# Kernel optimization log

Hardware: AMD Instinct MI355X
Metric: run time of the kernel (lower is better)

Reference implementation:

```python
import jax, jax.numpy as jnp
import numpy as np


def _conv(x, w, b, dilation=1):
    # NHWC input, HWIO kernel, SAME padding, optional dilation (TF Conv2D semantics)
    y = jax.lax.conv_general_dilated(
        x, w, window_strides=(1, 1), padding='SAME',
        rhs_dilation=(dilation, dilation),
        dimension_numbers=('NHWC', 'HWIO', 'NHWC'))
    return y + b


def _grid_pool(x, row_loc, col_loc):
    # Irregular-grid mean pool + broadcast back (tf resize of a 1x1 cell == broadcast).
    # Vectorized as two normalized one-hot contractions instead of per-cell loops.
    B, H, W, C = x.shape
    M = row_loc.shape[0] - 1
    N = col_loc.shape[0] - 1
    row_ids = jnp.searchsorted(row_loc, jnp.arange(H), side='right') - 1  # [H] in [0,M)
    col_ids = jnp.searchsorted(col_loc, jnp.arange(W), side='right') - 1  # [W] in [0,N)
    Rm = jax.nn.one_hot(row_ids, M, dtype=x.dtype).T            # [M,H]
    Cm = jax.nn.one_hot(col_ids, N, dtype=x.dtype)              # [W,N]
    Rm = Rm / jnp.sum(Rm, axis=1, keepdims=True)                # row-mean weights
    Cm = Cm / jnp.sum(Cm, axis=0, keepdims=True)                # col-mean weights
    pooled = jnp.einsum('mh,bhwc,wn->bmnc', Rm, x, Cm)          # per-cell means [B,M,N,C]
    return pooled[:, row_ids][:, :, col_ids]                    # broadcast back [B,H,W,C]


def setup_inputs() -> dict:
    key = jax.random.key(0)
    ks = jax.random.split(key, 8)
    B, H, W, Cin = 2, 1024, 1024, 18
    inp = {
        'input': jax.random.normal(ks[0], (B, H, W, Cin), dtype=jnp.float32),
        'row_loc': (jnp.arange(17, dtype=jnp.int32) * (H // 16)),  # 16 irregular-capable cells, endpoints 0..H
        'col_loc': (jnp.arange(17, dtype=jnp.int32) * (W // 16)),
        'w1': jax.random.normal(ks[1], (3, 3, Cin, 6), dtype=jnp.float32) * 0.1,
        'b1': jnp.zeros((6,), jnp.float32),
        'w2': jax.random.normal(ks[2], (3, 3, Cin, 6), dtype=jnp.float32) * 0.1,
        'b2': jnp.zeros((6,), jnp.float32),
        'w3': jax.random.normal(ks[3], (3, 3, Cin, 6), dtype=jnp.float32) * 0.1,
        'b3': jnp.zeros((6,), jnp.float32),
        'wb1': jax.random.normal(ks[4], (1, 1, 18, 18), dtype=jnp.float32) * 0.1,
        'bb1': jnp.zeros((18,), jnp.float32),
        'wb2': jax.random.normal(ks[5], (1, 1, 18, 1), dtype=jnp.float32) * 0.1,
        'bb2': jnp.zeros((1,), jnp.float32),
    }
    return inp


def reference(input, row_loc, col_loc, w1, b1, w2, b2, w3, b3, wb1, bb1, wb2, bb2):
    c1 = jax.nn.relu(_conv(input, w1, b1, 1))
    c2 = jax.nn.relu(_conv(input, w2, b2, 2))
    c3 = jax.nn.relu(_conv(input, w3, b3, 3))
    c = jnp.concatenate([c1, c2, c3], axis=3)          # [B,H,W,18]
    branch1 = jax.nn.relu(_conv(c, wb1, bb1, 1))       # [B,H,W,18]
    branch1 = _grid_pool(branch1, row_loc, col_loc)
    branch2 = _conv(c, wb2, bb2, 1)                    # [B,H,W,1]
    branch2 = _grid_pool(branch2, row_loc, col_loc)
    branch2 = jax.nn.sigmoid(branch2)
    output = jnp.concatenate([branch1, c, branch2], axis=3)  # [B,H,W,37]
    return (output, branch2)
```

## Files before the change

### kernel.cpp

```cpp
#include <hip/hip_runtime.h>
#include <math.h>

typedef _Float16 f16;
typedef _Float16 f16x2 __attribute__((ext_vector_type(2)));
typedef _Float16 f16x8 __attribute__((ext_vector_type(8)));
typedef float    f32x4 __attribute__((ext_vector_type(4)));

static constexpr int B = 2, H = 1024, W = 1024;
static constexpr int NCELL = 16;
static constexpr unsigned TOTAL1 = 2u*1024u*1024u*37u;

static constexpr size_t WT_OFF   = 0;
static constexpr size_t WBT_OFF  = 21504;
static constexpr size_t BIAS_OFF = 23552;
static constexpr size_t CWS_OFF  = 32768;
static constexpr size_t SUMS_OFF = CWS_OFF + (size_t)8192*9216;
static constexpr size_t P1_OFF   = SUMS_OFF + 9728*4;
static constexpr size_t P2_OFF   = P1_OFF + 9216*4;
static constexpr size_t RID_OFF  = P2_OFF + 512*4;
static constexpr size_t CID_OFF  = RID_OFF + 1024*4;

__device__ __forceinline__ int cell_of(const int* __restrict__ loc, int x) {
    int id = 0;
#pragma unroll
    for (int i = 1; i < NCELL; ++i) id = (loc[i] <= x) ? i : id;
    return id;
}

__global__ __launch_bounds__(256)
void prep(const float* __restrict__ w1, const float* __restrict__ b1,
          const float* __restrict__ w2, const float* __restrict__ b2,
          const float* __restrict__ w3, const float* __restrict__ b3,
          const float* __restrict__ wb1, const float* __restrict__ bb1,
          const float* __restrict__ wb2, const float* __restrict__ bb2,
          f16* __restrict__ wT, f16* __restrict__ wbT, float* __restrict__ biasPad)
{
    const int tid = threadIdx.x;
    for (int t = tid; t < 10752; t += 256) {
        int cv = t / 3584, r = t - cv*3584;
        int co = r / 224,  k = r - co*224;
        float val = 0.f;
        if (k < 216 && co < 6) {
            int tap = k / 24, ci = k - tap*24;
            if (ci < 18) {
                const float* wsrc = cv==0 ? w1 : cv==1 ? w2 : w3;
                val = wsrc[(tap*18 + ci)*6 + co];
            }
        }
        wT[t] = (f16)val;
    }
    for (int t = tid; t < 1024; t += 256) {
        int nt = t >> 9, r = t & 511;
        int colv = r >> 5, ci = r & 31;
        int co2 = nt*16 + colv;
        float val = 0.f;
        if (ci < 18) {
            if (co2 < 18) val = wb1[ci*18 + co2];
            else if (co2 == 18) val = wb2[ci];
        }
        wbT[t] = (f16)val;
    }
    for (int t = tid; t < 80; t += 256) {
        float val = 0.f;
        if (t < 48) { int cv = t >> 4, co = t & 15;
            const float* bp = cv==0 ? b1 : cv==1 ? b2 : b3;
            val = (co < 6) ? bp[co] : 0.f; }
        else if (t < 64) val = bb1[t - 48];
        else { int c = t - 64;
            val = (c==0) ? bb1[16] : (c==1) ? bb1[17] : (c==2) ? bb2[0] : 0.f; }
        biasPad[t] = val;
    }
}

__global__ __launch_bounds__(256)
void conv_mfma(const float* __restrict__ in,
               const f16* __restrict__ wT, const f16* __restrict__ wbT,
               const float* __restrict__ biasPad,
               const int* __restrict__ row_loc, const int* __restrict__ col_loc,
               f16* __restrict__ c_ws, float* __restrict__ sums)
{
    __shared__ __align__(16) f16 s_a[22*22*24];
    __shared__ float s_red[4][19];

    const int tid = threadIdx.x;
    const int bx  = blockIdx.x;
    const int b   = bx >> 12, rem = bx & 4095;
    const int h0  = (rem >> 6) * 16, w0 = (rem & 63) * 16;

    const int gh0 = h0 - 3, gw0 = w0 - 3;
    const bool interior = (gh0 >= 0) && (h0 + 19 <= H) && (gw0 >= 0) && (w0 + 19 <= W);
#pragma unroll
    for (int k = 0; k < 2; ++k) {
        const int p = tid + k*256;
        if (p < 484) {
            const int r = p / 22, cc = p - r*22;
            const int gh = gh0 + r, gw = gw0 + cc;
            const bool ok = interior || ((unsigned)gh < (unsigned)H && (unsigned)gw < (unsigned)W);
            float2 L[9];
            if (ok) {
                const float* sp = in + ((size_t)((size_t)b*H + gh)*W + gw)*18;
#pragma unroll
                for (int j = 0; j < 9; ++j) L[j] = *(const float2*)(sp + 2*j);
            } else {
#pragma unroll
                for (int j = 0; j < 9; ++j) L[j] = make_float2(0.f, 0.f);
            }
            f16x8 A0, A1, A2;
#pragma unroll
            for (int j = 0; j < 4; ++j) { A0[2*j] = (f16)L[j].x;   A0[2*j+1] = (f16)L[j].y; }
#pragma unroll
            for (int j = 0; j < 4; ++j) { A1[2*j] = (f16)L[4+j].x; A1[2*j+1] = (f16)L[4+j].y; }
            A2[0] = (f16)L[8].x; A2[1] = (f16)L[8].y;
#pragma unroll
            for (int j = 2; j < 8; ++j) A2[j] = (f16)0.f;
            *(f16x8*)&s_a[p*24 + 0]  = A0;
            *(f16x8*)&s_a[p*24 + 8]  = A1;
            *(f16x8*)&s_a[p*24 + 16] = A2;
        }
    }
    __syncthreads();

    const int lane = tid & 63, wv = tid >> 6;
    const int lm = lane & 15, g = lane >> 4;

    f32x4 acc[3][4];
#pragma unroll
    for (int cv = 0; cv < 3; ++cv)
#pragma unroll
        for (int mt = 0; mt < 4; ++mt) acc[cv][mt] = (f32x4){0.f,0.f,0.f,0.f};

#pragma unroll
    for (int cv = 0; cv < 3; ++cv) {
        const int d = cv + 1;
        const f16* wtc = wT + cv*3584 + lm*224 + g*8;
        f16x8 bf[7];
#pragma unroll
        for (int kb = 0; kb < 7; ++kb) bf[kb] = *(const f16x8*)(wtc + kb*32);
        int tofs[7];
#pragma unroll
        for (int kb = 0; kb < 7; ++kb) {
            int i8 = kb*4 + g; if (i8 > 26) i8 = 26;
            int tap = i8 / 3;
            int ci0 = (i8 - tap*3) * 8;
            int ky = tap / 3, kx = tap - ky*3;
            tofs[kb] = (((ky-1)*d)*22 + (kx-1)*d)*24 + ci0;
        }
#pragma unroll
        for (int mt = 0; mt < 4; ++mt) {
            const int py = wv*4 + mt;
            const int base = ((py + 3)*22 + lm + 3) * 24;
            f32x4 a = acc[cv][mt];
#pragma unroll
            for (int kb = 0; kb < 7; ++kb) {
                f16x8 af = *(const f16x8*)&s_a[base + tofs[kb]];
                a = __builtin_amdgcn_mfma_f32_16x16x32_f16(af, bf[kb], a, 0, 0, 0);
            }
            acc[cv][mt] = a;
        }
    }

    __syncthreads();
    f16* ct = s_a;
    const float bs0 = biasPad[lm], bs1 = biasPad[16 + lm], bs2 = biasPad[32 + lm];
    const bool act = (lm < 6);
#pragma unroll
    for (int cv = 0; cv < 3; ++cv) {
        const float bv = cv==0 ? bs0 : cv==1 ? bs1 : bs2;
#pragma unroll
        for (int mt = 0; mt < 4; ++mt) {
            const int py = wv*4 + mt;
#pragma unroll
            for (int r = 0; r < 4; ++r) {
                float val = fmaxf(acc[cv][mt][r] + bv, 0.f);
                const int px = g*4 + r;
                if (act) ct[(py*16 + px)*18 + cv*6 + lm] = (f16)val;
            }
        }
    }
    __syncthreads();

    {
        const f16x8* src = (const f16x8*)ct;
        f16x8* dst = (f16x8*)(c_ws + (size_t)bx * 4608);
#pragma unroll
        for (int k = 0; k < 3; ++k) {
            const int i = tid + k*256;
            if (i < 576) dst[i] = src[i];
        }
    }

    const f16x8 wbf0 = *(const f16x8*)(wbT + lm*32 + g*8);
    const f16x8 wbf1 = *(const f16x8*)(wbT + (16 + lm)*32 + g*8);
    const f32x4 z4 = (f32x4){0.f,0.f,0.f,0.f};
    const unsigned* ctu = (const unsigned*)ct;
    f32x4 acc2[4][2];
#pragma unroll
    for (int mt = 0; mt < 4; ++mt) {
        const int py = wv*4 + mt;
        const int du = ((py*16 + lm)*36 + g*16) >> 2;
        union { f16x8 v; unsigned u[4]; } A;
#pragma unroll
        for (int j = 0; j < 4; ++j) A.u[j] = ctu[du + j];
        acc2[mt][0] = __builtin_amdgcn_mfma_f32_16x16x32_f16(A.v, wbf0, z4, 0, 0, 0);
        acc2[mt][1] = __builtin_amdgcn_mfma_f32_16x16x32_f16(A.v, wbf1, z4, 0, 0, 0);
    }

    const float bb0 = biasPad[48 + lm];
    const float bb1v = biasPad[64 + lm];
    const int rid0 = cell_of(row_loc, h0), rid1 = cell_of(row_loc, h0 + 15);
    const int cid0 = cell_of(col_loc, w0), cid1 = cell_of(col_loc, w0 + 15);
    if (rid0 == rid1 && cid0 == cid1) {
        float ps0 = 0.f, ps1 = 0.f;
#pragma unroll
        for (int mt = 0; mt < 4; ++mt)
#pragma unroll
            for (int r = 0; r < 4; ++r) {
                float v0 = fmaxf(acc2[mt][0][r] + bb0, 0.f);
                float t1 = acc2[mt][1][r] + bb1v;
                float v1x = (lm < 2) ? fmaxf(t1, 0.f) : t1;
                ps0 += v0; ps1 += v1x;
            }
        ps0 += __shfl_xor(ps0, 16); ps0 += __shfl_xor(ps0, 32);
        ps1 += __shfl_xor(ps1, 16); ps1 += __shfl_xor(ps1, 32);
        if (lane < 16) s_red[wv][lane] = ps0;
        if (lane < 3)  s_red[wv][16 + lane] = ps1;
        __syncthreads();
        if (tid < 19) {
            float s = s_red[0][tid] + s_red[1][tid] + s_red[2][tid] + s_red[3][tid];
            const int cell = b*256 + rid0*16 + cid0;
            atomicAdd(&sums[cell*19 + tid], s);
        }
    } else {
#pragma unroll
        for (int mt = 0; mt < 4; ++mt) {
            const int py = wv*4 + mt;
            const int rid = cell_of(row_loc, h0 + py);
#pragma unroll
            for (int r = 0; r < 4; ++r) {
                const int px = g*4 + r;
                const int cell = b*256 + rid*16 + cell_of(col_loc, w0 + px);
                float v0 = fmaxf(acc2[mt][0][r] + bb0, 0.f);
                atomicAdd(&sums[cell*19 + lm], v0);
                if (lm < 3) {
                    float t1 = acc2[mt][1][r] + bb1v;
                    float v1x = (lm < 2) ? fmaxf(t1, 0.f) : t1;
                    atomicAdd(&sums[cell*19 + 16 + lm], v1x);
                }
            }
        }
    }
}

__global__ __launch_bounds__(256)
void finalize(const int* __restrict__ row_loc, const int* __restrict__ col_loc,
              const float* __restrict__ sums,
              float* __restrict__ pooled1, float* __restrict__ pooled2,
              int* __restrict__ row_ids, int* __restrict__ col_ids)
{
    __shared__ int rcnt[NCELL], ccnt[NCELL];
    const int tid = threadIdx.x;
    if (tid < NCELL) { rcnt[tid] = 0; ccnt[tid] = 0; }
    __syncthreads();
    for (int h = tid; h < H; h += 256) {
        int r = cell_of(row_loc, h); row_ids[h] = r; atomicAdd(&rcnt[r], 1);
    }
    for (int w = tid; w < W; w += 256) {
        int cc = cell_of(col_loc, w); col_ids[w] = cc; atomicAdd(&ccnt[cc], 1);
    }
    __syncthreads();
    for (int t = tid; t < B*256*18; t += 256) {
        int cell = t / 18, ch = t - cell*18;
        int rid = (cell >> 4) & 15, cid = cell & 15;
        int cnt = rcnt[rid] * ccnt[cid];
        pooled1[t] = (cnt > 0) ? sums[cell*19 + ch] / (float)cnt : 0.f;
    }
    for (int t = tid; t < B*256; t += 256) {
        int rid = (t >> 4) & 15, cid = t & 15;
        int cnt = rcnt[rid] * ccnt[cid];
        float v = (cnt > 0) ? sums[t*19 + 18] / (float)cnt : 0.f;
        pooled2[t] = 1.f / (1.f + __expf(-v));
    }
}

__global__ __launch_bounds__(256)
void assemble(const f16* __restrict__ c_ws, const float* __restrict__ pooled1,
              const float* __restrict__ pooled2, const int* __restrict__ row_ids,
              const int* __restrict__ col_ids, float* __restrict__ out)
{
    __shared__ __align__(16) f16 s_c[1024*18];
    __shared__ float s_p1[16*18];
    __shared__ float s_p2[16];
    __shared__ unsigned char s_cid[1024];

    const int tid = threadIdx.x;
    const int bx  = blockIdx.x;
    const int b   = bx >> 10, h = bx & 1023;

    const int tbase = b*4096 + (h >> 4)*64;
    const size_t rofs = (size_t)(h & 15) * 576;
    const char* cbase = (const char*)c_ws;
    float4* dstv = (float4*)s_c;
#pragma unroll
    for (int k = 0; k < 9; ++k) {
        const int j = tid + k*256;
        const int t = j / 36, i = j - t*36;
        const float4 v = *(const float4*)(cbase + (size_t)(tbase + t)*9216 + rofs + (size_t)i*16);
        dstv[j] = v;
    }
    const int rid = row_ids[h];
    for (int i = tid; i < 288; i += 256) {
        int cid = i / 18, ch = i - cid*18;
        s_p1[i] = pooled1[((size_t)(b*256 + rid*16 + cid))*18 + ch];
    }
    if (tid < 16) s_p2[tid] = pooled2[b*256 + rid*16 + tid];
    for (int i = tid; i < 1024; i += 256) s_cid[i] = (unsigned char)col_ids[i];
    __syncthreads();

    float* orow = out + (size_t)bx * (1024*37);
    for (int i4 = tid; i4 < 1024*37/4; i4 += 256) {
        const int o0 = i4*4;
        float v[4];
#pragma unroll
        for (int j = 0; j < 4; ++j) {
            const int o = o0 + j;
            const unsigned pix = (unsigned)o / 37u;
            const int ch = o - (int)pix*37;
            const int cid = s_cid[pix];
            float val;
            if (ch < 18)       val = s_p1[cid*18 + ch];
            else if (ch < 36)  val = (float)s_c[pix*18 + (ch - 18)];
            else               val = s_p2[cid];
            v[j] = val;
        }
        *(float4*)(orow + o0) = make_float4(v[0], v[1], v[2], v[3]);
    }
    float* o2 = out + (size_t)TOTAL1 + (size_t)bx * 1024;
    {
        const int p0 = tid * 4;
        float4 v = make_float4(s_p2[s_cid[p0]], s_p2[s_cid[p0+1]],
                               s_p2[s_cid[p0+2]], s_p2[s_cid[p0+3]]);
        *(float4*)(o2 + p0) = v;
    }
}

extern "C" void kernel_launch(void* const* d_in, const int* in_sizes, int n_in,
                              void* d_out, int out_size, void* d_ws, size_t ws_size,
                              hipStream_t stream)
{
    (void)in_sizes; (void)n_in; (void)out_size; (void)ws_size;
    const float* in      = (const float*)d_in[0];
    const int*   row_loc = (const int*)d_in[1];
    const int*   col_loc = (const int*)d_in[2];
    const float *w1 = (const float*)d_in[3],  *b1  = (const float*)d_in[4];
    const float *w2 = (const float*)d_in[5],  *b2  = (const float*)d_in[6];
    const float *w3 = (const float*)d_in[7],  *b3  = (const float*)d_in[8];
    const float *wb1= (const float*)d_in[9],  *bb1 = (const float*)d_in[10];
    const float *wb2= (const float*)d_in[11], *bb2 = (const float*)d_in[12];

    float* out = (float*)d_out;
    char*  ws  = (char*)d_ws;

    f16*   wT      = (f16*)(ws + WT_OFF);
    f16*   wbT     = (f16*)(ws + WBT_OFF);
    float* biasPad = (float*)(ws + BIAS_OFF);
    f16*   c_ws    = (f16*)(ws + CWS_OFF);
    float* sums    = (float*)(ws + SUMS_OFF);
    float* pooled1 = (float*)(ws + P1_OFF);
    float* pooled2 = (float*)(ws + P2_OFF);
    int*   row_ids = (int*)(ws + RID_OFF);
    int*   col_ids = (int*)(ws + CID_OFF);

    prep<<<dim3(1), dim3(256), 0, stream>>>(w1, b1, w2, b2, w3, b3,
                                            wb1, bb1, wb2, bb2, wT, wbT, biasPad);
    (void)hipMemsetAsync(sums, 0, 9728*sizeof(float), stream);

    conv_mfma<<<dim3(8192), dim3(256), 0, stream>>>(
        in, wT, wbT, biasPad, row_loc, col_loc, c_ws, sums);

    finalize<<<dim3(1), dim3(256), 0, stream>>>(
        row_loc, col_loc, sums, pooled1, pooled2, row_ids, col_ids);

    assemble<<<dim3(B*H), dim3(256), 0, stream>>>(
        c_ws, pooled1, pooled2, row_ids, col_ids, out);
}
```

Before: 210.9 us.

## Process four tiles per block with double-buffered register prefetch of halo loads

After: 413.4 us. +96.0%, slower.

```diff
diff --git a/kernel.cpp b/kernel.cpp
--- a/kernel.cpp
+++ b/kernel.cpp
@@ -9,6 +9,9 @@
 static constexpr int B = 2, H = 1024, W = 1024;
 static constexpr int NCELL = 16;
 static constexpr unsigned TOTAL1 = 2u*1024u*1024u*37u;
+
+static constexpr int NT_PER_BLK = 4;
+static constexpr int NBLK = 8192 / NT_PER_BLK;
 
 static constexpr size_t WT_OFF   = 0;
 static constexpr size_t WBT_OFF  = 21504;
@@ -27,15 +30,46 @@
     return id;
 }
 
+struct PxRegs { float2 v[9]; };
+
+__device__ __forceinline__ void issue_load(PxRegs& P, const float* __restrict__ in,
+                                           int b, int gh, int gw) {
+    const bool ok = ((unsigned)gh < (unsigned)H) && ((unsigned)gw < (unsigned)W);
+    if (ok) {
+        const float* sp = in + ((size_t)((size_t)b*H + gh)*W + gw)*18;
+#pragma unroll
+        for (int j = 0; j < 9; ++j) P.v[j] = *(const float2*)(sp + 2*j);
+    } else {
+#pragma unroll
+        for (int j = 0; j < 9; ++j) P.v[j] = make_float2(0.f, 0.f);
+    }
+}
+
+__device__ __forceinline__ void stage_write(f16* __restrict__ sa, const PxRegs& P, int p) {
+    f16x8 A0, A1, A2;
+#pragma unroll
+    for (int j = 0; j < 4; ++j) { A0[2*j] = (f16)P.v[j].x;   A0[2*j+1] = (f16)P.v[j].y; }
+#pragma unroll
+    for (int j = 0; j < 4; ++j) { A1[2*j] = (f16)P.v[4+j].x; A1[2*j+1] = (f16)P.v[4+j].y; }
+    A2[0] = (f16)P.v[8].x; A2[1] = (f16)P.v[8].y;
+#pragma unroll
+    for (int j = 2; j < 8; ++j) A2[j] = (f16)0.f;
+    *(f16x8*)&sa[p*24 + 0]  = A0;
+    *(f16x8*)&sa[p*24 + 8]  = A1;
+    *(f16x8*)&sa[p*24 + 16] = A2;
+}
+
 __global__ __launch_bounds__(256)
 void prep(const float* __restrict__ w1, const float* __restrict__ b1,
           const float* __restrict__ w2, const float* __restrict__ b2,
           const float* __restrict__ w3, const float* __restrict__ b3,
           const float* __restrict__ wb1, const float* __restrict__ bb1,
           const float* __restrict__ wb2, const float* __restrict__ bb2,
-          f16* __restrict__ wT, f16* __restrict__ wbT, float* __restrict__ biasPad)
+          f16* __restrict__ wT, f16* __restrict__ wbT, float* __restrict__ biasPad,
+          float* __restrict__ sums)
 {
     const int tid = threadIdx.x;
+    for (int t = tid; t < 9728; t += 256) sums[t] = 0.f;
     for (int t = tid; t < 10752; t += 256) {
         int cv = t / 3584, r = t - cv*3584;
         int co = r / 224,  k = r - co*224;
@@ -72,181 +106,174 @@
     }
 }
 
-__global__ __launch_bounds__(256)
+__global__ __launch_bounds__(256, 3)
 void conv_mfma(const float* __restrict__ in,
                const f16* __restrict__ wT, const f16* __restrict__ wbT,
                const float* __restrict__ biasPad,
                const int* __restrict__ row_loc, const int* __restrict__ col_loc,
                f16* __restrict__ c_ws, float* __restrict__ sums)
 {
-    __shared__ __align__(16) f16 s_a[22*22*24];
+    __shared__ __align__(16) f16 s_a[2][484*24];
     __shared__ float s_red[4][19];
 
     const int tid = threadIdx.x;
-    const int bx  = blockIdx.x;
-    const int b   = bx >> 12, rem = bx & 4095;
-    const int h0  = (rem >> 6) * 16, w0 = (rem & 63) * 16;
-
-    const int gh0 = h0 - 3, gw0 = w0 - 3;
-    const bool interior = (gh0 >= 0) && (h0 + 19 <= H) && (gw0 >= 0) && (w0 + 19 <= W);
-#pragma unroll
-    for (int k = 0; k < 2; ++k) {
-        const int p = tid + k*256;
-        if (p < 484) {
-            const int r = p / 22, cc = p - r*22;
-            const int gh = gh0 + r, gw = gw0 + cc;
-            const bool ok = interior || ((unsigned)gh < (unsigned)H && (unsigned)gw < (unsigned)W);
-            float2 L[9];
-            if (ok) {
-                const float* sp = in + ((size_t)((size_t)b*H + gh)*W + gw)*18;
-#pragma unroll
-                for (int j = 0; j < 9; ++j) L[j] = *(const float2*)(sp + 2*j);
-            } else {
-#pragma unroll
-                for (int j = 0; j < 9; ++j) L[j] = make_float2(0.f, 0.f);
-            }
-            f16x8 A0, A1, A2;
-#pragma unroll
-            for (int j = 0; j < 4; ++j) { A0[2*j] = (f16)L[j].x;   A0[2*j+1] = (f16)L[j].y; }
-#pragma unroll
-            for (int j = 0; j < 4; ++j) { A1[2*j] = (f16)L[4+j].x; A1[2*j+1] = (f16)L[4+j].y; }
-            A2[0] = (f16)L[8].x; A2[1] = (f16)L[8].y;
-#pragma unroll
-            for (int j = 2; j < 8; ++j) A2[j] = (f16)0.f;
-            *(f16x8*)&s_a[p*24 + 0]  = A0;
-            *(f16x8*)&s_a[p*24 + 8]  = A1;
-            *(f16x8*)&s_a[p*24 + 16] = A2;
-        }
-    }
-    __syncthreads();
+    const int s   = blockIdx.x;
+    const int b   = s >> 10, rr = s & 1023;
+    const int h0  = (rr >> 4) * 16;
+    const int wbase = (rr & 15) * 64;
+
+    const int p0 = tid, p1 = tid + 256;
+    const int r0 = p0 / 22, c0 = p0 - r0*22;
+    const int r1 = p1 / 22, c1 = p1 - r1*22;
+    const bool has1 = (tid < 228);
 
     const int lane = tid & 63, wv = tid >> 6;
     const int lm = lane & 15, g = lane >> 4;
 
-    f32x4 acc[3][4];
-#pragma unroll
-    for (int cv = 0; cv < 3; ++cv)
-#pragma unroll
-        for (int mt = 0; mt < 4; ++mt) acc[cv][mt] = (f32x4){0.f,0.f,0.f,0.f};
-
-#pragma unroll
-    for (int cv = 0; cv < 3; ++cv) {
-        const int d = cv + 1;
-        const f16* wtc = wT + cv*3584 + lm*224 + g*8;
-        f16x8 bf[7];
-#pragma unroll
-        for (int kb = 0; kb < 7; ++kb) bf[kb] = *(const f16x8*)(wtc + kb*32);
-        int tofs[7];
-#pragma unroll
-        for (int kb = 0; kb < 7; ++kb) {
-            int i8 = kb*4 + g; if (i8 > 26) i8 = 26;
-            int tap = i8 / 3;
-            int ci0 = (i8 - tap*3) * 8;
-            int ky = tap / 3, kx = tap - ky*3;
-            tofs[kb] = (((ky-1)*d)*22 + (kx-1)*d)*24 + ci0;
-        }
+    PxRegs P[2][2];
+    issue_load(P[0][0], in, b, h0 - 3 + r0, wbase - 3 + c0);
+    if (has1) issue_load(P[0][1], in, b, h0 - 3 + r1, wbase - 3 + c1);
+
+#pragma unroll
+    for (int t = 0; t < NT_PER_BLK; ++t) {
+        const int w0 = wbase + t*16;
+        f16* sa = s_a[t & 1];
+
+        stage_write(sa, P[t & 1][0], p0);
+        if (has1) stage_write(sa, P[t & 1][1], p1);
+        if (t < NT_PER_BLK - 1) {
+            issue_load(P[(t+1) & 1][0], in, b, h0 - 3 + r0, w0 + 16 - 3 + c0);
+            if (has1) issue_load(P[(t+1) & 1][1], in, b, h0 - 3 + r1, w0 + 16 - 3 + c1);
+        }
+        __syncthreads();
+
+        f32x4 acc[3][4];
+#pragma unroll
+        for (int cv = 0; cv < 3; ++cv)
+#pragma unroll
+            for (int mt = 0; mt < 4; ++mt) acc[cv][mt] = (f32x4){0.f,0.f,0.f,0.f};
+
+#pragma unroll
+        for (int cv = 0; cv < 3; ++cv) {
+            const int d = cv + 1;
+            const f16* wtc = wT + cv*3584 + lm*224 + g*8;
+            f16x8 bf[7];
+#pragma unroll
+            for (int kb = 0; kb < 7; ++kb) bf[kb] = *(const f16x8*)(wtc + kb*32);
+            int tofs[7];
+#pragma unroll
+            for (int kb = 0; kb < 7; ++kb) {
+                int i8 = kb*4 + g; if (i8 > 26) i8 = 26;
+                int tap = i8 / 3;
+                int ci0 = (i8 - tap*3) * 8;
+                int ky = tap / 3, kx = tap - ky*3;
+                tofs[kb] = (((ky-1)*d)*22 + (kx-1)*d)*24 + ci0;
+            }
+#pragma unroll
+            for (int mt = 0; mt < 4; ++mt) {
+                const int py = wv*4 + mt;
+                const int base = ((py + 3)*22 + lm + 3) * 24;
+                f32x4 a = acc[cv][mt];
+#pragma unroll
+                for (int kb = 0; kb < 7; ++kb) {
+                    f16x8 af = *(const f16x8*)&sa[base + tofs[kb]];
+                    a = __builtin_amdgcn_mfma_f32_16x16x32_f16(af, bf[kb], a, 0, 0, 0);
+                }
+                acc[cv][mt] = a;
+            }
+        }
+        __syncthreads();
+
+        f16* ct = sa;
+        const float bs0 = biasPad[lm], bs1 = biasPad[16 + lm], bs2 = biasPad[32 + lm];
+        const bool act = (lm < 6);
+#pragma unroll
+        for (int cv = 0; cv < 3; ++cv) {
+            const float bv = cv==0 ? bs0 : cv==1 ? bs1 : bs2;
+#pragma unroll
+            for (int mt = 0; mt < 4; ++mt) {
+                const int py = wv*4 + mt;
+#pragma unroll
+                for (int r = 0; r < 4; ++r) {
+                    float val = fmaxf(acc[cv][mt][r] + bv, 0.f);
+                    const int px = g*4 + r;
+                    if (act) ct[(py*16 + px)*18 + cv*6 + lm] = (f16)val;
+                }
+            }
+        }
+        __syncthreads();
+
+        const int tile_lin = b*4096 + (rr >> 4)*64 + (rr & 15)*4 + t;
+        {
+            const f16x8* src = (const f16x8*)ct;
+            f16x8* dst = (f16x8*)(c_ws + (size_t)tile_lin * 4608);
+#pragma unroll
+            for (int k = 0; k < 3; ++k) {
+                const int i = tid + k*256;
+                if (i < 576) dst[i] = src[i];
+            }
+        }
+
+        const f16x8 wbf0 = *(const f16x8*)(wbT + lm*32 + g*8);
+        const f16x8 wbf1 = *(const f16x8*)(wbT + (16 + lm)*32 + g*8);
+        const f32x4 z4 = (f32x4){0.f,0.f,0.f,0.f};
+        const unsigned* ctu = (const unsigned*)ct;
+        f32x4 acc2[4][2];
 #pragma unroll
         for (int mt = 0; mt < 4; ++mt) {
             const int py = wv*4 + mt;
-            const int base = ((py + 3)*22 + lm + 3) * 24;
-            f32x4 a = acc[cv][mt];
-#pragma unroll
-            for (int kb = 0; kb < 7; ++kb) {
-                f16x8 af = *(const f16x8*)&s_a[base + tofs[kb]];
-                a = __builtin_amdgcn_mfma_f32_16x16x32_f16(af, bf[kb], a, 0, 0, 0);
-            }
-            acc[cv][mt] = a;
-        }
-    }
-
-    __syncthreads();
-    f16* ct = s_a;
-    const float bs0 = biasPad[lm], bs1 = biasPad[16 + lm], bs2 = biasPad[32 + lm];
-    const bool act = (lm < 6);
-#pragma unroll
-    for (int cv = 0; cv < 3; ++cv) {
-        const float bv = cv==0 ? bs0 : cv==1 ? bs1 : bs2;
-#pragma unroll
-        for (int mt = 0; mt < 4; ++mt) {
-            const int py = wv*4 + mt;
-#pragma unroll
-            for (int r = 0; r < 4; ++r) {
-                float val = fmaxf(acc[cv][mt][r] + bv, 0.f);
-                const int px = g*4 + r;
-                if (act) ct[(py*16 + px)*18 + cv*6 + lm] = (f16)val;
-            }
-        }
-    }
-    __syncthreads();
-
-    {
-        const f16x8* src = (const f16x8*)ct;
-        f16x8* dst = (f16x8*)(c_ws + (size_t)bx * 4608);
-#pragma unroll
-        for (int k = 0; k < 3; ++k) {
-            const int i = tid + k*256;
-            if (i < 576) dst[i] = src[i];
-        }
-    }
-
-    const f16x8 wbf0 = *(const f16x8*)(wbT + lm*32 + g*8);
-    const f16x8 wbf1 = *(const f16x8*)(wbT + (16 + lm)*32 + g*8);
-    const f32x4 z4 = (f32x4){0.f,0.f,0.f,0.f};
-    const unsigned* ctu = (const unsigned*)ct;
-    f32x4 acc2[4][2];
-#pragma unroll
-    for (int mt = 0; mt < 4; ++mt) {
-        const int py = wv*4 + mt;
-        const int du = ((py*16 + lm)*36 + g*16) >> 2;
-        union { f16x8 v; unsigned u[4]; } A;
-#pragma unroll
-        for (int j = 0; j < 4; ++j) A.u[j] = ctu[du + j];
-        acc2[mt][0] = __builtin_amdgcn_mfma_f32_16x16x32_f16(A.v, wbf0, z4, 0, 0, 0);
-        acc2[mt][1] = __builtin_amdgcn_mfma_f32_16x16x32_f16(A.v, wbf1, z4, 0, 0, 0);
-    }
-
-    const float bb0 = biasPad[48 + lm];
-    const float bb1v = biasPad[64 + lm];
-    const int rid0 = cell_of(row_loc, h0), rid1 = cell_of(row_loc, h0 + 15);
-    const int cid0 = cell_of(col_loc, w0), cid1 = cell_of(col_loc, w0 + 15);
-    if (rid0 == rid1 && cid0 == cid1) {
-        float ps0 = 0.f, ps1 = 0.f;
-#pragma unroll
-        for (int mt = 0; mt < 4; ++mt)
-#pragma unroll
-            for (int r = 0; r < 4; ++r) {
-                float v0 = fmaxf(acc2[mt][0][r] + bb0, 0.f);
-                float t1 = acc2[mt][1][r] + bb1v;
-                float v1x = (lm < 2) ? fmaxf(t1, 0.f) : t1;
-                ps0 += v0; ps1 += v1x;
-            }
-        ps0 += __shfl_xor(ps0, 16); ps0 += __shfl_xor(ps0, 32);
-        ps1 += __shfl_xor(ps1, 16); ps1 += __shfl_xor(ps1, 32);
-        if (lane < 16) s_red[wv][lane] = ps0;
-        if (lane < 3)  s_red[wv][16 + lane] = ps1;
-        __syncthreads();
-        if (tid < 19) {
-            float s = s_red[0][tid] + s_red[1][tid] + s_red[2][tid] + s_red[3][tid];
-            const int cell = b*256 + rid0*16 + cid0;
-            atomicAdd(&sums[cell*19 + tid], s);
-        }
-    } else {
-#pragma unroll
-        for (int mt = 0; mt < 4; ++mt) {
-            const int py = wv*4 + mt;
-            const int rid = cell_of(row_loc, h0 + py);
-#pragma unroll
-            for (int r = 0; r < 4; ++r) {
-                const int px = g*4 + r;
-                const int cell = b*256 + rid*16 + cell_of(col_loc, w0 + px);
-                float v0 = fmaxf(acc2[mt][0][r] + bb0, 0.f);
-                atomicAdd(&sums[cell*19 + lm], v0);
-                if (lm < 3) {
+            const int du = ((py*16 + lm)*36 + g*16) >> 2;
+            union { f16x8 v; unsigned u[4]; } A;
+#pragma unroll
+            for (int j = 0; j < 4; ++j) A.u[j] = ctu[du + j];
+            acc2[mt][0] = __builtin_amdgcn_mfma_f32_16x16x32_f16(A.v, wbf0, z4, 0, 0, 0);
+            acc2[mt][1] = __builtin_amdgcn_mfma_f32_16x16x32_f16(A.v, wbf1, z4, 0, 0, 0);
+        }
+
+        const float bb0 = biasPad[48 + lm];
+        const float bb1v = biasPad[64 + lm];
+        const int rid0 = cell_of(row_loc, h0), rid1 = cell_of(row_loc, h0 + 15);
+        const int cid0 = cell_of(col_loc, w0), cid1 = cell_of(col_loc, w0 + 15);
+        if (rid0 == rid1 && cid0 == cid1) {
+            float ps0 = 0.f, ps1 = 0.f;
+#pragma unroll
+            for (int mt = 0; mt < 4; ++mt)
+#pragma unroll
+                for (int r = 0; r < 4; ++r) {
+                    float v0 = fmaxf(acc2[mt][0][r] + bb0, 0.f);
                     float t1 = acc2[mt][1][r] + bb1v;
                     float v1x = (lm < 2) ? fmaxf(t1, 0.f) : t1;
-                    atomicAdd(&sums[cell*19 + 16 + lm], v1x);
+                    ps0 += v0; ps1 += v1x;
                 }
-            }
+            ps0 += __shfl_xor(ps0, 16); ps0 += __shfl_xor(ps0, 32);
+            ps1 += __shfl_xor(ps1, 16); ps1 += __shfl_xor(ps1, 32);
+            if (lane < 16) s_red[wv][lane] = ps0;
+            if (lane < 3)  s_red[wv][16 + lane] = ps1;
+            __syncthreads();
+            if (tid < 19) {
+                float ssum = s_red[0][tid] + s_red[1][tid] + s_red[2][tid] + s_red[3][tid];
+                const int cell = b*256 + rid0*16 + cid0;
+                atomicAdd(&sums[cell*19 + tid], ssum);
+            }
+        } else {
+#pragma unroll
+            for (int mt = 0; mt < 4; ++mt) {
+                const int py = wv*4 + mt;
+                const int rid = cell_of(row_loc, h0 + py);
+#pragma unroll
+                for (int r = 0; r < 4; ++r) {
+                    const int px = g*4 + r;
+                    const int cell = b*256 + rid*16 + cell_of(col_loc, w0 + px);
+                    float v0 = fmaxf(acc2[mt][0][r] + bb0, 0.f);
+                    atomicAdd(&sums[cell*19 + lm], v0);
+                    if (lm < 3) {
+                        float t1 = acc2[mt][1][r] + bb1v;
+                        float v1x = (lm < 2) ? fmaxf(t1, 0.f) : t1;
+                        atomicAdd(&sums[cell*19 + 16 + lm], v1x);
+                    }
+                }
+            }
+            __syncthreads();
         }
     }
 }
@@ -371,10 +398,9 @@
     int*   col_ids = (int*)(ws + CID_OFF);
 
     prep<<<dim3(1), dim3(256), 0, stream>>>(w1, b1, w2, b2, w3, b3,
-                                            wb1, bb1, wb2, bb2, wT, wbT, biasPad);
-    (void)hipMemsetAsync(sums, 0, 9728*sizeof(float), stream);
-
-    conv_mfma<<<dim3(8192), dim3(256), 0, stream>>>(
+                                            wb1, bb1, wb2, bb2, wT, wbT, biasPad, sums);
+
+    conv_mfma<<<dim3(NBLK), dim3(256), 0, stream>>>(
         in, wT, wbT, biasPad, row_loc, col_loc, c_ws, sums);
 
     finalize<<<dim3(1), dim3(256), 0, stream>>>(
```

## Pad LDS tile layout to cut bank conflicts, swizzle block order, fold memset

Applied to the files above, without the earlier changes.

After: 214.8 us. Within noise of the previous version (+1.9%).

```diff
diff --git a/kernel.cpp b/kernel.cpp
--- a/kernel.cpp
+++ b/kernel.cpp
@@ -20,6 +20,8 @@
 static constexpr size_t RID_OFF  = P2_OFF + 512*4;
 static constexpr size_t CID_OFF  = RID_OFF + 1024*4;
 
+__device__ __forceinline__ int slot_ofs(int px) { return px*48 + ((px >> 3) << 4); }
+
 __device__ __forceinline__ int cell_of(const int* __restrict__ loc, int x) {
     int id = 0;
 #pragma unroll
@@ -33,9 +35,11 @@
           const float* __restrict__ w3, const float* __restrict__ b3,
           const float* __restrict__ wb1, const float* __restrict__ bb1,
           const float* __restrict__ wb2, const float* __restrict__ bb2,
-          f16* __restrict__ wT, f16* __restrict__ wbT, float* __restrict__ biasPad)
+          f16* __restrict__ wT, f16* __restrict__ wbT, float* __restrict__ biasPad,
+          float* __restrict__ sums)
 {
     const int tid = threadIdx.x;
+    for (int t = tid; t < 9728; t += 256) sums[t] = 0.f;
     for (int t = tid; t < 10752; t += 256) {
         int cv = t / 3584, r = t - cv*3584;
         int co = r / 224,  k = r - co*224;
@@ -79,11 +83,11 @@
                const int* __restrict__ row_loc, const int* __restrict__ col_loc,
                f16* __restrict__ c_ws, float* __restrict__ sums)
 {
-    __shared__ __align__(16) f16 s_a[22*22*24];
+    __shared__ __align__(16) f16 s_a[12096];
     __shared__ float s_red[4][19];
 
     const int tid = threadIdx.x;
-    const int bx  = blockIdx.x;
+    const int bx  = (int)(blockIdx.x & 7)*1024 + (int)(blockIdx.x >> 3);
     const int b   = bx >> 12, rem = bx & 4095;
     const int h0  = (rem >> 6) * 16, w0 = (rem & 63) * 16;
 
@@ -113,9 +117,10 @@
             A2[0] = (f16)L[8].x; A2[1] = (f16)L[8].y;
 #pragma unroll
             for (int j = 2; j < 8; ++j) A2[j] = (f16)0.f;
-            *(f16x8*)&s_a[p*24 + 0]  = A0;
-            *(f16x8*)&s_a[p*24 + 8]  = A1;
-            *(f16x8*)&s_a[p*24 + 16] = A2;
+            char* sb = (char*)s_a + slot_ofs(p);
+            *(f16x8*)(sb)      = A0;
+            *(f16x8*)(sb + 16) = A1;
+            *(f16x8*)(sb + 32) = A2;
         }
     }
     __syncthreads();
@@ -136,23 +141,24 @@
         f16x8 bf[7];
 #pragma unroll
         for (int kb = 0; kb < 7; ++kb) bf[kb] = *(const f16x8*)(wtc + kb*32);
-        int tofs[7];
+        int dpx[7], cib[7];
 #pragma unroll
         for (int kb = 0; kb < 7; ++kb) {
             int i8 = kb*4 + g; if (i8 > 26) i8 = 26;
             int tap = i8 / 3;
-            int ci0 = (i8 - tap*3) * 8;
             int ky = tap / 3, kx = tap - ky*3;
-            tofs[kb] = (((ky-1)*d)*22 + (kx-1)*d)*24 + ci0;
+            dpx[kb] = ((ky-1)*d)*22 + (kx-1)*d;
+            cib[kb] = (i8 - tap*3) * 16;
         }
 #pragma unroll
         for (int mt = 0; mt < 4; ++mt) {
             const int py = wv*4 + mt;
-            const int base = ((py + 3)*22 + lm + 3) * 24;
+            const int pxrow = (py + 3)*22 + lm + 3;
             f32x4 a = acc[cv][mt];
 #pragma unroll
             for (int kb = 0; kb < 7; ++kb) {
-                f16x8 af = *(const f16x8*)&s_a[base + tofs[kb]];
+                const int px = pxrow + dpx[kb];
+                f16x8 af = *(const f16x8*)((const char*)s_a + slot_ofs(px) + cib[kb]);
                 a = __builtin_amdgcn_mfma_f32_16x16x32_f16(af, bf[kb], a, 0, 0, 0);
             }
             acc[cv][mt] = a;
@@ -371,8 +377,7 @@
     int*   col_ids = (int*)(ws + CID_OFF);
 
     prep<<<dim3(1), dim3(256), 0, stream>>>(w1, b1, w2, b2, w3, b3,
-                                            wb1, bb1, wb2, bb2, wT, wbT, biasPad);
-    (void)hipMemsetAsync(sums, 0, 9728*sizeof(float), stream);
+                                            wb1, bb1, wb2, bb2, wT, wbT, biasPad, sums);
 
     conv_mfma<<<dim3(8192), dim3(256), 0, stream>>>(
         in, wT, wbT, biasPad, row_loc, col_loc, c_ws, sums);
```
